# Performance work log

Hardware: AMD Instinct MI355X
Metric: run time of the kernel (lower is better)

## Reference

```python
import jax, jax.numpy as jnp
import numpy as np
import math

N_HEAD = 12


def setup_inputs() -> dict:
    key = jax.random.key(0)
    k1, k2, k3 = jax.random.split(key, 3)
    B, T, C = 4, 2048, 768
    x = jax.random.normal(k1, (B, T, C), dtype=jnp.float32)
    W = jax.random.normal(k2, (C, 3 * C), dtype=jnp.float32) * 0.02
    b = jax.random.normal(k3, (3 * C,), dtype=jnp.float32) * 0.02
    return {"x": x, "W": W, "b": b}


def reference(x, W, b):
    B, T, C = x.shape
    H = N_HEAD
    d = C // H
    qkv = x @ W + b                                # [B,T,3C]
    q, k, v = jnp.split(qkv, 3, axis=-1)           # each [B,T,C]
    q = q.reshape(B, T, H, d).transpose(0, 2, 1, 3)  # [B,H,T,d]
    k = k.reshape(B, T, H, d).transpose(0, 2, 1, 3)
    v = v.reshape(B, T, H, d).transpose(0, 2, 1, 3)
    # NOTE: source multiplies by sqrt(d) (not divides) -- faithful reproduction.
    att = jnp.einsum('bhqd,bhkd->bhqk', q, k) * (1.0 * math.sqrt(d))
    causal = jnp.tril(jnp.ones((T, T), dtype=bool))  # [T,T]
    att = jnp.where(causal[None, None, :, :], att, -jnp.inf)
    att = jax.nn.softmax(att, axis=-1)
    y = jnp.einsum('bhqk,bhkd->bhqd', att, v)      # [B,H,T,d]
    y = y.transpose(0, 2, 1, 3).reshape(B, T, C)   # [B,T,C]
    return y
```

## Files before the change

kernel.cpp:

```cpp
#include <hip/hip_runtime.h>
#include <math.h>

#define B_ 4
#define T_ 2048
#define C_ 768
#define H_ 12
#define D_ 64
#define N3C (3*C_)
#define BH_ (B_*H_)
#define QSCALE 11.5415603f
#define PPS 72

typedef float f32x4 __attribute__((ext_vector_type(4)));
typedef _Float16 f16x8 __attribute__((ext_vector_type(8)));
typedef unsigned short ushort_t;

__device__ __forceinline__ void async16(const void* g, void* l) {
    __builtin_amdgcn_global_load_lds(
        (const __attribute__((address_space(1))) unsigned int*)(g),
        (__attribute__((address_space(3))) unsigned int*)(l),
        16, 0, 0);
}

__device__ __forceinline__ unsigned pk_f16(float a, float b) {
    __fp16 r2[2];
    *(__fp16 __attribute__((ext_vector_type(2)))*)r2 = __builtin_amdgcn_cvt_pkrtz(a, b);
    return *(unsigned*)r2;
}

__global__ __launch_bounds__(256) void conv_x(const float* __restrict__ x,
                                              _Float16* __restrict__ Xh)
{
    int idx = blockIdx.x * 256 + threadIdx.x;
    const float4 a = *reinterpret_cast<const float4*>(&x[(size_t)idx * 8]);
    const float4 b = *reinterpret_cast<const float4*>(&x[(size_t)idx * 8 + 4]);
    f16x8 o = {(_Float16)a.x, (_Float16)a.y, (_Float16)a.z, (_Float16)a.w,
               (_Float16)b.x, (_Float16)b.y, (_Float16)b.z, (_Float16)b.w};
    *reinterpret_cast<f16x8*>(&Xh[(size_t)idx * 8]) = o;
}

__global__ __launch_bounds__(256) void conv_w(const float* __restrict__ W,
                                              _Float16* __restrict__ Wh)
{
    __shared__ float tile[64][65];
    int n0 = blockIdx.x * 64, k0 = blockIdx.y * 64;
    int tid = threadIdx.x;
    #pragma unroll
    for (int t = 0; t < 16; ++t) {
        int c = t * 256 + tid;
        int kr = c >> 6, nc = c & 63;
        tile[kr][nc] = W[(size_t)(k0 + kr) * N3C + n0 + nc];
    }
    __syncthreads();
    #pragma unroll
    for (int t = 0; t < 16; ++t) {
        int c = t * 256 + tid;
        int nr = c >> 6, kc = c & 63;
        Wh[(size_t)(n0 + nr) * C_ + k0 + kc] = (_Float16)tile[kc][nr];
    }
}

__global__ __launch_bounds__(256) void qkv_gemm(const _Float16* __restrict__ Xh,
                                                const _Float16* __restrict__ Wh,
                                                const float* __restrict__ bias,
                                                _Float16* __restrict__ Qf,
                                                _Float16* __restrict__ Kf,
                                                _Float16* __restrict__ Vt)
{
    __shared__ __align__(16) ushort_t As[128 * 64];
    __shared__ __align__(16) ushort_t Bs[128 * 64];

    int tid = threadIdx.x, lane = tid & 63, w = tid >> 6;
    int wm = w >> 1, wn = w & 1;
    int l15 = lane & 15, l4 = lane >> 4;
    int srow = lane >> 3;
    int scol = (((lane & 7) ^ srow)) << 3;

    int wg = blockIdx.x;
    int l = (wg & 7) * 144 + (wg >> 3);
    int mt = l / 18, nt = l % 18;
    int row0 = mt * 128, col0 = nt * 128;

    f32x4 acc[4][4];
    #pragma unroll
    for (int i = 0; i < 4; ++i)
        #pragma unroll
        for (int j = 0; j < 4; ++j)
            acc[i][j] = f32x4{0.f, 0.f, 0.f, 0.f};

    const char* AsC = (const char*)As;
    const char* BsC = (const char*)Bs;

    for (int k0 = 0; k0 < C_; k0 += 64) {
        __syncthreads();
        #pragma unroll
        for (int j = 0; j < 4; ++j) {
            int rowb = w * 32 + j * 8;
            async16(Xh + (size_t)(row0 + rowb + srow) * C_ + k0 + scol, &As[rowb * 64]);
            async16(Wh + (size_t)(col0 + rowb + srow) * C_ + k0 + scol, &Bs[rowb * 64]);
        }
        __syncthreads();

        #pragma unroll
        for (int kk = 0; kk < 2; ++kk) {
            f16x8 af[4], bfr[4];
            #pragma unroll
            for (int m = 0; m < 4; ++m) {
                int r = wm * 64 + m * 16 + l15;
                af[m] = *reinterpret_cast<const f16x8*>(AsC + r * 128 + ((kk * 64 + l4 * 16) ^ ((r & 7) << 4)));
            }
            #pragma unroll
            for (int n = 0; n < 4; ++n) {
                int r = wn * 64 + n * 16 + l15;
                bfr[n] = *reinterpret_cast<const f16x8*>(BsC + r * 128 + ((kk * 64 + l4 * 16) ^ ((r & 7) << 4)));
            }
            #pragma unroll
            for (int m = 0; m < 4; ++m)
                #pragma unroll
                for (int n = 0; n < 4; ++n)
                    acc[m][n] = __builtin_amdgcn_mfma_f32_16x16x32_f16(af[m], bfr[n], acc[m][n], 0, 0, 0);
        }
    }

    #pragma unroll
    for (int n = 0; n < 4; ++n) {
        int gcol = col0 + wn * 64 + n * 16 + l15;
        int p    = gcol / C_;
        int rem  = gcol - p * C_;
        int h    = rem >> 6, d = rem & 63;
        float bv = bias[gcol];
        #pragma unroll
        for (int m = 0; m < 4; ++m) {
            #pragma unroll
            for (int r = 0; r < 4; ++r) {
                int grow = row0 + wm * 64 + m * 16 + l4 * 4 + r;
                int b = grow >> 11, t = grow & (T_ - 1);
                int bh = b * H_ + h;
                float v = acc[m][n][r] + bv;
                if (p == 0) {
                    Qf[((size_t)bh * T_ + t) * D_ + d] = (_Float16)(v * QSCALE);
                } else if (p == 1) {
                    Kf[((size_t)bh * T_ + t) * D_ + d] = (_Float16)v;
                } else {
                    Vt[((size_t)bh * D_ + d) * T_ + t] = (_Float16)v;
                }
            }
        }
    }
}

__global__ __launch_bounds__(256) void attn(const _Float16* __restrict__ Qf,
                                            const _Float16* __restrict__ Kf,
                                            const _Float16* __restrict__ Vt,
                                            float* __restrict__ out)
{
    __shared__ __align__(16) char smem[41984];
    ushort_t* lds = (ushort_t*)smem;

    int tid = threadIdx.x, lane = tid & 63, w = tid >> 6;
    int l15 = lane & 15, l4 = lane >> 4;
    int bid = blockIdx.x;
    int qt = 15 - bid / BH_;
    int bh = bid % BH_;
    int b = bh / H_, h = bh % H_;
    int q0 = qt * 128;
    int ntile = 2 * qt + 2;

    f16x8 qf[2][2];
    #pragma unroll
    for (int qs = 0; qs < 2; ++qs) {
        int q = q0 + w * 32 + qs * 16 + l15;
        const _Float16* ph = Qf + ((size_t)bh * T_ + q) * D_;
        qf[qs][0] = *reinterpret_cast<const f16x8*>(ph + l4 * 8);
        qf[qs][1] = *reinterpret_cast<const f16x8*>(ph + 32 + l4 * 8);
    }

    f32x4 yacc[2][4];
    #pragma unroll
    for (int qs = 0; qs < 2; ++qs)
        #pragma unroll
        for (int dt = 0; dt < 4; ++dt)
            yacc[qs][dt] = f32x4{0.f, 0.f, 0.f, 0.f};
    float m_run[2] = {-INFINITY, -INFINITY};
    float l_run[2] = {0.f, 0.f};

    int srow = lane >> 3;
    int scol = ((lane & 7) ^ srow) << 3;
    ushort_t* Pw = lds + 16384 + w * (16 * PPS);
    const size_t kbase = (size_t)bh * T_;
    const size_t vbase = (size_t)bh * D_;

    #pragma unroll
    for (int j = 0; j < 2; ++j) {
        int row = (w * 2 + j) * 8 + srow;
        ushort_t* dK = lds + (w * 2 + j) * 512;
        async16(Kf + (kbase + row) * D_ + scol, dK);
        async16(Vt + (vbase + row) * T_ + scol, dK + 4096);
    }
    __syncthreads();

    int cur = 0;
    for (int it = 0; it < ntile; ++it) {
        int k0 = it * 64;
        int nxt = cur ^ 1;
        if (it + 1 < ntile) {
            int k0n = k0 + 64;
            #pragma unroll
            for (int j = 0; j < 2; ++j) {
                int row = (w * 2 + j) * 8 + srow;
                ushort_t* dK = lds + nxt * 8192 + (w * 2 + j) * 512;
                async16(Kf + (kbase + k0n + row) * D_ + scol, dK);
                async16(Vt + (vbase + row) * T_ + k0n + scol, dK + 4096);
            }
        }

        if (k0 <= q0 + w * 32 + 31) {
            const char* KHc = (const char*)(lds + cur * 8192);
            const char* VSc = KHc + 8192;
            f16x8 pa[2][2];

            #pragma unroll
            for (int qs = 0; qs < 2; ++qs) {
                f32x4 sa[4];
                #pragma unroll
                for (int i = 0; i < 4; ++i) sa[i] = f32x4{0.f, 0.f, 0.f, 0.f};

                __builtin_amdgcn_s_setprio(1);
                #pragma unroll
                for (int kt = 0; kt < 4; ++kt) {
                    int krow = kt * 16 + l15;
                    int swz = (krow & 7) << 4;
                    #pragma unroll
                    for (int dh = 0; dh < 2; ++dh) {
                        f16x8 kf = *reinterpret_cast<const f16x8*>(KHc + krow * 128 + ((dh * 64 + l4 * 16) ^ swz));
                        sa[kt] = __builtin_amdgcn_mfma_f32_16x16x32_f16(kf, qf[qs][dh], sa[kt], 0, 0, 0);
                    }
                }
                __builtin_amdgcn_s_setprio(0);

                if (it >= ntile - 2) {
                    int qg = q0 + w * 32 + qs * 16 + l15;
                    #pragma unroll
                    for (int kt = 0; kt < 4; ++kt)
                        #pragma unroll
                        for (int r = 0; r < 4; ++r)
                            if (k0 + kt * 16 + l4 * 4 + r > qg) sa[kt][r] = -INFINITY;
                }

                float mx = sa[0][0];
                #pragma unroll
                for (int kt = 0; kt < 4; ++kt)
                    #pragma unroll
                    for (int r = 0; r < 4; ++r) mx = fmaxf(mx, sa[kt][r]);
                mx = fmaxf(mx, __shfl_xor(mx, 16));
                mx = fmaxf(mx, __shfl_xor(mx, 32));

                float mn;
                if (__all(mx <= m_run[qs] + 8.0f)) {
                    mn = m_run[qs];
                } else {
                    mn = fmaxf(m_run[qs], mx);
                    float sc = exp2f(m_run[qs] - mn);
                    m_run[qs] = mn;
                    l_run[qs] *= sc;
                    #pragma unroll
                    for (int dt = 0; dt < 4; ++dt) yacc[qs][dt] *= sc;
                }

                float p[4][4];
                float rs = 0.f;
                #pragma unroll
                for (int kt = 0; kt < 4; ++kt)
                    #pragma unroll
                    for (int r = 0; r < 4; ++r) {
                        p[kt][r] = exp2f(sa[kt][r] - mn);
                        rs += p[kt][r];
                    }
                rs += __shfl_xor(rs, 16);
                rs += __shfl_xor(rs, 32);
                l_run[qs] += rs;

                int pb = l15 * PPS + l4 * 4;
                #pragma unroll
                for (int kt = 0; kt < 4; ++kt) {
                    *reinterpret_cast<unsigned*>(Pw + pb + kt * 16) = pk_f16(p[kt][0], p[kt][1]);
                    *reinterpret_cast<unsigned*>(Pw + pb + kt * 16 + 2) = pk_f16(p[kt][2], p[kt][3]);
                }
                pa[qs][0] = *reinterpret_cast<const f16x8*>(Pw + l15 * PPS + l4 * 8);
                pa[qs][1] = *reinterpret_cast<const f16x8*>(Pw + l15 * PPS + 32 + l4 * 8);
            }

            __builtin_amdgcn_s_setprio(1);
            #pragma unroll
            for (int dt = 0; dt < 4; ++dt) {
                int vrow = dt * 16 + l15;
                int vswz = (vrow & 7) << 4;
                #pragma unroll
                for (int kk = 0; kk < 2; ++kk) {
                    f16x8 vf = *reinterpret_cast<const f16x8*>(VSc + vrow * 128 + ((kk * 64 + l4 * 16) ^ vswz));
                    yacc[0][dt] = __builtin_amdgcn_mfma_f32_16x16x32_f16(vf, pa[0][kk], yacc[0][dt], 0, 0, 0);
                    yacc[1][dt] = __builtin_amdgcn_mfma_f32_16x16x32_f16(vf, pa[1][kk], yacc[1][dt], 0, 0, 0);
                }
            }
            __builtin_amdgcn_s_setprio(0);
        }
        __syncthreads();
        cur = nxt;
    }

    float* ot = (float*)smem;
    #pragma unroll
    for (int qs = 0; qs < 2; ++qs) {
        float inv = 1.0f / l_run[qs];
        int rq = w * 32 + qs * 16 + l15;
        #pragma unroll
        for (int dt = 0; dt < 4; ++dt)
            #pragma unroll
            for (int r = 0; r < 4; ++r)
                ot[rq * 68 + dt * 16 + l4 * 4 + r] = yacc[qs][dt][r] * inv;
    }
    __syncthreads();
    int rr = tid >> 1, c0 = (tid & 1) * 32;
    size_t ob = ((size_t)(b * T_ + q0 + rr)) * C_ + h * D_ + c0;
    #pragma unroll
    for (int u = 0; u < 8; ++u) {
        float4 v = *reinterpret_cast<const float4*>(&ot[rr * 68 + c0 + u * 4]);
        *reinterpret_cast<float4*>(&out[ob + u * 4]) = v;
    }
}

extern "C" void kernel_launch(void* const* d_in, const int* in_sizes, int n_in,
                              void* d_out, int out_size, void* d_ws, size_t ws_size,
                              hipStream_t stream)
{
    const float* x    = (const float*)d_in[0];
    const float* W    = (const float*)d_in[1];
    const float* bias = (const float*)d_in[2];

    const size_t per = (size_t)BH_ * T_ * D_;
    _Float16* Qf = (_Float16*)d_ws;
    _Float16* Kf = Qf + per;
    _Float16* Vt = Kf + per;
    _Float16* Xh = Vt + per;
    _Float16* Wh = Xh + (size_t)8192 * C_;

    conv_x<<<dim3((8192 * 768 / 8) / 256), 256, 0, stream>>>(x, Xh);
    conv_w<<<dim3(N3C / 64, C_ / 64), 256, 0, stream>>>(W, Wh);
    qkv_gemm<<<dim3(64 * 18), 256, 0, stream>>>(Xh, Wh, bias, Qf, Kf, Vt);
    attn<<<dim3(BH_ * (T_ / 128)), 256, 0, stream>>>(Qf, Kf, Vt, (float*)d_out);
}
```

Baseline: 149.8 us.

## Split long causal attention query tiles into two KV chunks with a merge kernel

After: 152.3 us. About the same (+1.7%).

```diff
diff --git a/kernel.cpp b/kernel.cpp
--- a/kernel.cpp
+++ b/kernel.cpp
@@ -149,10 +149,15 @@
     }
 }
 
+__device__ const unsigned char ITEM_QT[24] = {15,15,7,14,14,13,13,6,12,12,11,11,5,10,10,9,9,4,8,8,3,2,1,0};
+__device__ const unsigned char ITEM_CH[24] = { 0, 1,0, 0, 1, 0, 1,0, 0, 1, 0, 1,0, 0, 1,0,1,0,0,1,0,0,0,0};
+
 __global__ __launch_bounds__(256) void attn(const _Float16* __restrict__ Qf,
                                             const _Float16* __restrict__ Kf,
                                             const _Float16* __restrict__ Vt,
-                                            float* __restrict__ out)
+                                            float* __restrict__ out,
+                                            float* __restrict__ Op,
+                                            float* __restrict__ ML)
 {
     __shared__ __align__(16) char smem[41984];
     ushort_t* lds = (ushort_t*)smem;
@@ -160,11 +165,15 @@
     int tid = threadIdx.x, lane = tid & 63, w = tid >> 6;
     int l15 = lane & 15, l4 = lane >> 4;
     int bid = blockIdx.x;
-    int qt = 15 - bid / BH_;
+    int rank = bid / BH_;
     int bh = bid % BH_;
+    int qt = ITEM_QT[rank];
+    int ch = ITEM_CH[rank];
     int b = bh / H_, h = bh % H_;
     int q0 = qt * 128;
-    int ntile = 2 * qt + 2;
+
+    int it0 = (qt < 8 || ch == 0) ? 0 : (qt + 1);
+    int it1 = (qt >= 8 && ch == 0) ? (qt + 1) : (2 * qt + 2);
 
     f16x8 qf[2][2];
     #pragma unroll
@@ -190,20 +199,23 @@
     const size_t kbase = (size_t)bh * T_;
     const size_t vbase = (size_t)bh * D_;
 
-    #pragma unroll
-    for (int j = 0; j < 2; ++j) {
-        int row = (w * 2 + j) * 8 + srow;
-        ushort_t* dK = lds + (w * 2 + j) * 512;
-        async16(Kf + (kbase + row) * D_ + scol, dK);
-        async16(Vt + (vbase + row) * T_ + scol, dK + 4096);
+    {
+        int k00 = it0 * 64;
+        #pragma unroll
+        for (int j = 0; j < 2; ++j) {
+            int row = (w * 2 + j) * 8 + srow;
+            ushort_t* dK = lds + (w * 2 + j) * 512;
+            async16(Kf + (kbase + k00 + row) * D_ + scol, dK);
+            async16(Vt + (vbase + row) * T_ + k00 + scol, dK + 4096);
+        }
     }
     __syncthreads();
 
     int cur = 0;
-    for (int it = 0; it < ntile; ++it) {
+    for (int it = it0; it < it1; ++it) {
         int k0 = it * 64;
         int nxt = cur ^ 1;
-        if (it + 1 < ntile) {
+        if (it + 1 < it1) {
             int k0n = k0 + 64;
             #pragma unroll
             for (int j = 0; j < 2; ++j) {
@@ -238,7 +250,7 @@
                 }
                 __builtin_amdgcn_s_setprio(0);
 
-                if (it >= ntile - 2) {
+                if (it >= 2 * qt) {
                     int qg = q0 + w * 32 + qs * 16 + l15;
                     #pragma unroll
                     for (int kt = 0; kt < 4; ++kt)
@@ -309,24 +321,82 @@
     }
 
     float* ot = (float*)smem;
-    #pragma unroll
-    for (int qs = 0; qs < 2; ++qs) {
-        float inv = 1.0f / l_run[qs];
-        int rq = w * 32 + qs * 16 + l15;
-        #pragma unroll
-        for (int dt = 0; dt < 4; ++dt)
-            #pragma unroll
-            for (int r = 0; r < 4; ++r)
-                ot[rq * 68 + dt * 16 + l4 * 4 + r] = yacc[qs][dt][r] * inv;
-    }
-    __syncthreads();
-    int rr = tid >> 1, c0 = (tid & 1) * 32;
-    size_t ob = ((size_t)(b * T_ + q0 + rr)) * C_ + h * D_ + c0;
-    #pragma unroll
-    for (int u = 0; u < 8; ++u) {
-        float4 v = *reinterpret_cast<const float4*>(&ot[rr * 68 + c0 + u * 4]);
-        *reinterpret_cast<float4*>(&out[ob + u * 4]) = v;
-    }
+    if (qt < 8) {
+        #pragma unroll
+        for (int qs = 0; qs < 2; ++qs) {
+            float inv = 1.0f / l_run[qs];
+            int rq = w * 32 + qs * 16 + l15;
+            #pragma unroll
+            for (int dt = 0; dt < 4; ++dt)
+                #pragma unroll
+                for (int r = 0; r < 4; ++r)
+                    ot[rq * 68 + dt * 16 + l4 * 4 + r] = yacc[qs][dt][r] * inv;
+        }
+        __syncthreads();
+        int rr = tid >> 1, c0 = (tid & 1) * 32;
+        size_t ob = ((size_t)(b * T_ + q0 + rr)) * C_ + h * D_ + c0;
+        #pragma unroll
+        for (int u = 0; u < 8; ++u) {
+            float4 v = *reinterpret_cast<const float4*>(&ot[rr * 68 + c0 + u * 4]);
+            *reinterpret_cast<float4*>(&out[ob + u * 4]) = v;
+        }
+    } else {
+        #pragma unroll
+        for (int qs = 0; qs < 2; ++qs) {
+            int rq = w * 32 + qs * 16 + l15;
+            #pragma unroll
+            for (int dt = 0; dt < 4; ++dt)
+                #pragma unroll
+                for (int r = 0; r < 4; ++r)
+                    ot[rq * 68 + dt * 16 + l4 * 4 + r] = yacc[qs][dt][r];
+        }
+        if (l4 == 0) {
+            float* mlp = ML + (((size_t)bh * 8 + (qt - 8)) * 2 + ch) * 256;
+            #pragma unroll
+            for (int qs = 0; qs < 2; ++qs) {
+                int ql = w * 32 + qs * 16 + l15;
+                mlp[ql] = m_run[qs];
+                mlp[128 + ql] = l_run[qs];
+            }
+        }
+        __syncthreads();
+        int rr = tid >> 1, c0 = (tid & 1) * 32;
+        float* dst = Op + (((size_t)bh * 8 + (qt - 8)) * 2 + ch) * 8192 + rr * 64 + c0;
+        #pragma unroll
+        for (int u = 0; u < 8; ++u) {
+            float4 v = *reinterpret_cast<const float4*>(&ot[rr * 68 + c0 + u * 4]);
+            *reinterpret_cast<float4*>(&dst[u * 4]) = v;
+        }
+    }
+}
+
+__global__ __launch_bounds__(256) void merge(const float* __restrict__ Op,
+                                             const float* __restrict__ ML,
+                                             float* __restrict__ out)
+{
+    int gid = blockIdx.x * 256 + threadIdx.x;
+    int row = gid >> 4, seg = gid & 15;
+    int q = row & 127, qt8 = (row >> 7) & 7, bh = row >> 10;
+
+    size_t mbase = ((size_t)bh * 8 + qt8) * 2 * 256;
+    float m1 = ML[mbase + q],       l1 = ML[mbase + 128 + q];
+    float m2 = ML[mbase + 256 + q], l2 = ML[mbase + 256 + 128 + q];
+    float m = fmaxf(m1, m2);
+    float a1 = exp2f(m1 - m), a2 = exp2f(m2 - m);
+    float inv = 1.0f / (l1 * a1 + l2 * a2);
+
+    size_t obase = ((size_t)bh * 8 + qt8) * 2 * 8192 + q * 64 + seg * 4;
+    float4 o1 = *reinterpret_cast<const float4*>(&Op[obase]);
+    float4 o2 = *reinterpret_cast<const float4*>(&Op[obase + 8192]);
+    float4 r;
+    r.x = (o1.x * a1 + o2.x * a2) * inv;
+    r.y = (o1.y * a1 + o2.y * a2) * inv;
+    r.z = (o1.z * a1 + o2.z * a2) * inv;
+    r.w = (o1.w * a1 + o2.w * a2) * inv;
+
+    int b = bh / H_, h = bh % H_;
+    int t = (qt8 + 8) * 128 + q;
+    *reinterpret_cast<float4*>(&out[((size_t)(b * T_ + t)) * C_ + h * D_ + seg * 4]) = r;
 }
 
 extern "C" void kernel_launch(void* const* d_in, const int* in_sizes, int n_in,
@@ -343,9 +413,12 @@
     _Float16* Vt = Kf + per;
     _Float16* Xh = Vt + per;
     _Float16* Wh = Xh + (size_t)8192 * C_;
+    float*    Op = (float*)(Wh + (size_t)N3C * C_);
+    float*    ML = Op + (size_t)48 * 8 * 2 * 8192;
 
     conv_x<<<dim3((8192 * 768 / 8) / 256), 256, 0, stream>>>(x, Xh);
     conv_w<<<dim3(N3C / 64, C_ / 64), 256, 0, stream>>>(W, Wh);
     qkv_gemm<<<dim3(64 * 18), 256, 0, stream>>>(Xh, Wh, bias, Qf, Kf, Vt);
-    attn<<<dim3(BH_ * (T_ / 128)), 256, 0, stream>>>(Qf, Kf, Vt, (float*)d_out);
-}
+    attn<<<dim3(24 * BH_), 256, 0, stream>>>(Qf, Kf, Vt, (float*)d_out, Op, ML);
+    merge<<<dim3(49152 * 16 / 256), 256, 0, stream>>>(Op, ML, (float*)d_out);
+}
```
